# Kernel optimization log

Measured on AMD Instinct MI355X. Metric: run time of the kernel, lower is better.

The kernel has to match this reference:

```python
import jax, jax.numpy as jnp
import numpy as np

D_MODEL = 512
EPS = 1e-5


def setup_inputs() -> dict:
    key = jax.random.key(0)
    k1, k2, k3 = jax.random.split(key, 3)
    B, N, D = 8, 2048, D_MODEL
    output = jax.random.normal(k1, (B, N, D), dtype=jnp.float32)
    # multiplicative 0/1 float mask over the [B, N, N] score matrix
    slf_attn_mask = jax.random.randint(k2, (B, N, N), 0, 2).astype(jnp.float32)
    # nn.Linear(d_model, d_model): weight [out, in], xavier-uniform; bias zeros-ish
    limit = float(np.sqrt(6.0 / (D + D)))
    W = jax.random.uniform(k3, (D, D), dtype=jnp.float32, minval=-limit, maxval=limit)
    b = jnp.zeros((D,), dtype=jnp.float32)
    return {"output": output, "slf_attn_mask": slf_attn_mask, "W": W, "b": b}


def reference(output, slf_attn_mask, W, b):
    temperature = jnp.asarray(D_MODEL, output.dtype) ** 0.5
    # scores: [B, N, N] = (q / temp) @ k^T, then multiplicative mask
    attn = jnp.einsum("bnd,bmd->bnm", output / temperature, output) * slf_attn_mask
    # F.normalize(p=2, dim=-1, eps=1e-5): x / max(||x||_2, eps)
    norm = jnp.sqrt(jnp.sum(attn * attn, axis=-1, keepdims=True))
    attn = attn / jnp.maximum(norm, EPS)
    # values: elu(Linear(output)), Linear uses W @ x + b with W [out, in]
    v = jax.nn.elu(jnp.einsum("bnd,ed->bne", output, W) + b)
    return jnp.einsum("bnm,bme->bne", attn, v)
```

## Files before the change

### kernel.cpp

```cpp
#include <hip/hip_runtime.h>
#include <hip/hip_bf16.h>

#define NSEQ 2048
#define DM 512
#define BATCH 8
#define GTOT (BATCH * NSEQ)
#define INV_T 0.044194173824159216f
#define EPSN 1e-5f

typedef __bf16 bf16_t;
typedef bf16_t bf16x8 __attribute__((ext_vector_type(8)));
typedef float f32x16 __attribute__((ext_vector_type(16)));
typedef unsigned short u16;
typedef unsigned int u32;

__device__ __forceinline__ u16 f2bf(float f) {
    u32 u = __builtin_bit_cast(u32, f);
    u32 r = (u + 0x7FFFu + ((u >> 16) & 1u)) >> 16;
    return (u16)r;
}

__device__ __forceinline__ void async16(const u16* g, u16* l) {
    __builtin_amdgcn_global_load_lds(
        (const __attribute__((address_space(1))) u32*)g,
        (__attribute__((address_space(3))) u32*)l, 16, 0, 0);
}

__device__ __forceinline__ bf16x8 fragld(const u16* t, int row, int kc) {
    return *(const bf16x8*)(t + row * 32 + ((kc ^ ((row >> 1) & 3)) << 3));
}

#define MFMA32(a, b, c) __builtin_amdgcn_mfma_f32_32x32x16_bf16(a, b, c, 0, 0, 0)
#define ROWOFF(reg, lh) (((reg) & 3) + 8 * ((reg) >> 2) + 4 * (lh))

#define STAGE(Ag, ldA, Bg, ldB, k0)                                              \
    do {                                                                         \
        async16((Ag) + (long)rA0 * (ldA) + (k0) + kcg * 8, Ab + u0 * 512 + lane * 8);        \
        async16((Ag) + (long)(rA0 + 16) * (ldA) + (k0) + kcg * 8, Ab + (u0 + 1) * 512 + lane * 8); \
        async16((Bg) + (long)rA0 * (ldB) + (k0) + kcg * 8, Bb + u0 * 512 + lane * 8);        \
        async16((Bg) + (long)(rA0 + 16) * (ldB) + (k0) + kcg * 8, Bb + (u0 + 1) * 512 + lane * 8); \
    } while (0)

__global__ __launch_bounds__(256) void k_convert(
    const float* __restrict__ X, const float* __restrict__ W,
    u16* __restrict__ Kbf, u16* __restrict__ Wbf, float* __restrict__ ssbuf) {
    const long NK = (long)GTOT * DM / 4;
    const long NW = (long)DM * DM / 4;
    const long NS = GTOT / 4;
    long i = (long)blockIdx.x * 256 + threadIdx.x;
    if (i < NK) {
        float4 f = ((const float4*)X)[i];
        ushort4 o;
        o.x = f2bf(f.x); o.y = f2bf(f.y); o.z = f2bf(f.z); o.w = f2bf(f.w);
        ((ushort4*)Kbf)[i] = o;
    } else if (i < NK + NW) {
        long j = i - NK;
        float4 f = ((const float4*)W)[j];
        ushort4 o;
        o.x = f2bf(f.x); o.y = f2bf(f.y); o.z = f2bf(f.z); o.w = f2bf(f.w);
        ((ushort4*)Wbf)[j] = o;
    } else if (i < NK + NW + NS) {
        ((float4*)ssbuf)[i - NK - NW] = (float4){0.f, 0.f, 0.f, 0.f};
    }
}

__global__ __launch_bounds__(256, 4) void k_vgemm(
    const u16* __restrict__ Wbf, const u16* __restrict__ Kbf,
    const float* __restrict__ bias, u16* __restrict__ vT) {
    __shared__ __attribute__((aligned(16))) u16 Ab[4096], Bb[4096];
    const int tid = threadIdx.x, wave = tid >> 6, lane = tid & 63;
    const int l31 = lane & 31, lh = lane >> 5;
    const int wy = wave >> 1, wx = wave & 1;
    const int M0 = blockIdx.y * 128, N0 = blockIdx.x * 128;
    const u16* Ag = Wbf + (long)M0 * DM;
    const u16* Bg = Kbf + (long)N0 * DM;

    const int u0 = wave * 2;
    const int rA0 = u0 * 16 + (lane >> 2);
    const int kcg = (lane & 3) ^ ((lane >> 3) & 3);

    f32x16 acc[2][2];
#pragma unroll
    for (int i = 0; i < 2; ++i)
#pragma unroll
        for (int j = 0; j < 2; ++j)
#pragma unroll
            for (int e = 0; e < 16; ++e) acc[i][j][e] = 0.f;

    for (int kt = 0; kt < 16; ++kt) {
        const int k0 = kt * 32;
        __syncthreads();
        STAGE(Ag, DM, Bg, DM, k0);
        __syncthreads();
#pragma unroll
        for (int ks = 0; ks < 2; ++ks) {
            int kc = ks * 2 + lh;
            bf16x8 a0 = fragld(Ab, wy * 64 + l31, kc);
            bf16x8 a1 = fragld(Ab, wy * 64 + 32 + l31, kc);
            bf16x8 b0 = fragld(Bb, wx * 64 + l31, kc);
            bf16x8 b1 = fragld(Bb, wx * 64 + 32 + l31, kc);
            acc[0][0] = MFMA32(a0, b0, acc[0][0]);
            acc[0][1] = MFMA32(a0, b1, acc[0][1]);
            acc[1][0] = MFMA32(a1, b0, acc[1][0]);
            acc[1][1] = MFMA32(a1, b1, acc[1][1]);
        }
    }
#pragma unroll
    for (int mi = 0; mi < 2; ++mi) {
#pragma unroll
        for (int reg = 0; reg < 16; ++reg) {
            int e = M0 + wy * 64 + mi * 32 + ROWOFF(reg, lh);
            float bv = bias[e];
#pragma unroll
            for (int ni = 0; ni < 2; ++ni) {
                int g = N0 + wx * 64 + ni * 32 + l31;
                float x = acc[mi][ni][reg] + bv;
                float v = x > 0.f ? x : (__expf(x) - 1.f);
                vT[(long)e * GTOT + g] = f2bf(v);
            }
        }
    }
}

__global__ __launch_bounds__(256, 4) void k_sgemm(
    const u16* __restrict__ Kbf, const float* __restrict__ mask,
    u16* __restrict__ Sbuf, float* __restrict__ ssbuf) {
    __shared__ __attribute__((aligned(16))) u16 Ab[4096], Bb[4096];
    const int tid = threadIdx.x, wave = tid >> 6, lane = tid & 63;
    const int l31 = lane & 31, lh = lane >> 5;
    const int wy = wave >> 1, wx = wave & 1;
    const int b = blockIdx.z;
    const int M0 = blockIdx.y * 128, N0 = blockIdx.x * 128;
    const u16* Ag = Kbf + (long)(b * NSEQ + M0) * DM;
    const u16* Bg = Kbf + (long)(b * NSEQ + N0) * DM;

    const int u0 = wave * 2;
    const int rA0 = u0 * 16 + (lane >> 2);
    const int kcg = (lane & 3) ^ ((lane >> 3) & 3);

    f32x16 acc[2][2];
#pragma unroll
    for (int i = 0; i < 2; ++i)
#pragma unroll
        for (int j = 0; j < 2; ++j)
#pragma unroll
            for (int e = 0; e < 16; ++e) acc[i][j][e] = 0.f;

    for (int kt = 0; kt < 16; ++kt) {
        const int k0 = kt * 32;
        __syncthreads();
        STAGE(Ag, DM, Bg, DM, k0);
        __syncthreads();
#pragma unroll
        for (int ks = 0; ks < 2; ++ks) {
            int kc = ks * 2 + lh;
            bf16x8 a0 = fragld(Ab, wy * 64 + l31, kc);
            bf16x8 a1 = fragld(Ab, wy * 64 + 32 + l31, kc);
            bf16x8 b0 = fragld(Bb, wx * 64 + l31, kc);
            bf16x8 b1 = fragld(Bb, wx * 64 + 32 + l31, kc);
            acc[0][0] = MFMA32(a0, b0, acc[0][0]);
            acc[0][1] = MFMA32(a0, b1, acc[0][1]);
            acc[1][0] = MFMA32(a1, b0, acc[1][0]);
            acc[1][1] = MFMA32(a1, b1, acc[1][1]);
        }
    }
#pragma unroll
    for (int mi = 0; mi < 2; ++mi) {
#pragma unroll
        for (int reg = 0; reg < 16; ++reg) {
            long rg = (long)b * NSEQ + M0 + wy * 64 + mi * 32 + ROWOFF(reg, lh);
            float v = 0.f;
#pragma unroll
            for (int ni = 0; ni < 2; ++ni) {
                int cg = N0 + wx * 64 + ni * 32 + l31;
                float s = acc[mi][ni][reg] * INV_T * mask[rg * NSEQ + cg];
                v += s * s;
                Sbuf[rg * NSEQ + cg] = f2bf(s);
            }
            v += __shfl_xor(v, 1, 32);
            v += __shfl_xor(v, 2, 32);
            v += __shfl_xor(v, 4, 32);
            v += __shfl_xor(v, 8, 32);
            v += __shfl_xor(v, 16, 32);
            if (l31 == 0) atomicAdd(&ssbuf[rg], v);
        }
    }
}

__global__ __launch_bounds__(256, 4) void k_pv(
    const u16* __restrict__ Sbuf, const u16* __restrict__ vT,
    const float* __restrict__ ssbuf, float* __restrict__ Out) {
    __shared__ __attribute__((aligned(16))) u16 Ab[4096], Bb[4096];
    __shared__ float sc[128];
    const int tid = threadIdx.x, wave = tid >> 6, lane = tid & 63;
    const int l31 = lane & 31, lh = lane >> 5;
    const int wy = wave >> 1, wx = wave & 1;
    const int b = blockIdx.z;
    const int M0 = blockIdx.y * 128, N0 = blockIdx.x * 128;
    const u16* Ag = Sbuf + (long)(b * NSEQ + M0) * NSEQ;
    const u16* Bg = vT + (long)N0 * GTOT + b * NSEQ;

    if (tid < 128) {
        float v = ssbuf[b * NSEQ + M0 + tid];
        sc[tid] = 1.f / fmaxf(sqrtf(v), EPSN);
    }

    const int u0 = wave * 2;
    const int rA0 = u0 * 16 + (lane >> 2);
    const int kcg = (lane & 3) ^ ((lane >> 3) & 3);

    f32x16 acc[2][2];
#pragma unroll
    for (int i = 0; i < 2; ++i)
#pragma unroll
        for (int j = 0; j < 2; ++j)
#pragma unroll
            for (int e = 0; e < 16; ++e) acc[i][j][e] = 0.f;

    for (int kt = 0; kt < 64; ++kt) {
        const int k0 = kt * 32;
        __syncthreads();
        STAGE(Ag, NSEQ, Bg, GTOT, k0);
        __syncthreads();
#pragma unroll
        for (int ks = 0; ks < 2; ++ks) {
            int kc = ks * 2 + lh;
            bf16x8 a0 = fragld(Ab, wy * 64 + l31, kc);
            bf16x8 a1 = fragld(Ab, wy * 64 + 32 + l31, kc);
            bf16x8 b0 = fragld(Bb, wx * 64 + l31, kc);
            bf16x8 b1 = fragld(Bb, wx * 64 + 32 + l31, kc);
            acc[0][0] = MFMA32(a0, b0, acc[0][0]);
            acc[0][1] = MFMA32(a0, b1, acc[0][1]);
            acc[1][0] = MFMA32(a1, b0, acc[1][0]);
            acc[1][1] = MFMA32(a1, b1, acc[1][1]);
        }
    }
#pragma unroll
    for (int mi = 0; mi < 2; ++mi) {
#pragma unroll
        for (int reg = 0; reg < 16; ++reg) {
            int rl = wy * 64 + mi * 32 + ROWOFF(reg, lh);
            float s = sc[rl];
            float* op = Out + ((long)b * NSEQ + M0 + rl) * DM;
#pragma unroll
            for (int ni = 0; ni < 2; ++ni) {
                int d = N0 + wx * 64 + ni * 32 + l31;
                op[d] = acc[mi][ni][reg] * s;
            }
        }
    }
}

extern "C" void kernel_launch(void* const* d_in, const int* in_sizes, int n_in,
                              void* d_out, int out_size, void* d_ws, size_t ws_size,
                              hipStream_t stream) {
    const float* X = (const float*)d_in[0];
    const float* mask = (const float*)d_in[1];
    const float* W = (const float*)d_in[2];
    const float* bias = (const float*)d_in[3];
    float* out = (float*)d_out;

    char* ws = (char*)d_ws;
    u16* Kbf = (u16*)ws;
    u16* Wbf = (u16*)(ws + 16777216);
    u16* vT = (u16*)(ws + 17301504);
    u16* Sbuf = (u16*)(ws + 34078720);
    float* ssbuf = (float*)(ws + 101187584);

    k_convert<<<8464, 256, 0, stream>>>(X, W, Kbf, Wbf, ssbuf);
    k_vgemm<<<dim3(128, 4), 256, 0, stream>>>(Wbf, Kbf, bias, vT);
    k_sgemm<<<dim3(16, 16, 8), 256, 0, stream>>>(Kbf, mask, Sbuf, ssbuf);
    k_pv<<<dim3(4, 16, 8), 256, 0, stream>>>(Sbuf, vT, ssbuf, out);
}
```

Measured before the change: 354.4 us.

## Double-buffer LDS staging in all GEMMs and enlarge score GEMM tiles

Every GEMM kernel now uses two LDS buffers. The next K-slice is loaded asynchronously while MFMAs run on the current one, which cuts the per-iteration barrier pair down to a single barrier. The score GEMM also moves from 128x128 tiles with 256 threads to 256x256 tiles with 512 threads, where each wave computes four by two MFMA blocks, so K tiles are reused more and global traffic drops. The cost is much larger LDS use (64KB per sgemm block) and more accumulator registers, which lowers occupancy.

```diff
diff --git a/kernel.cpp b/kernel.cpp
--- a/kernel.cpp
+++ b/kernel.cpp
@@ -32,14 +32,6 @@
 
 #define MFMA32(a, b, c) __builtin_amdgcn_mfma_f32_32x32x16_bf16(a, b, c, 0, 0, 0)
 #define ROWOFF(reg, lh) (((reg) & 3) + 8 * ((reg) >> 2) + 4 * (lh))
-
-#define STAGE(Ag, ldA, Bg, ldB, k0)                                              \
-    do {                                                                         \
-        async16((Ag) + (long)rA0 * (ldA) + (k0) + kcg * 8, Ab + u0 * 512 + lane * 8);        \
-        async16((Ag) + (long)(rA0 + 16) * (ldA) + (k0) + kcg * 8, Ab + (u0 + 1) * 512 + lane * 8); \
-        async16((Bg) + (long)rA0 * (ldB) + (k0) + kcg * 8, Bb + u0 * 512 + lane * 8);        \
-        async16((Bg) + (long)(rA0 + 16) * (ldB) + (k0) + kcg * 8, Bb + (u0 + 1) * 512 + lane * 8); \
-    } while (0)
 
 __global__ __launch_bounds__(256) void k_convert(
     const float* __restrict__ X, const float* __restrict__ W,
@@ -64,111 +56,72 @@
     }
 }
 
-__global__ __launch_bounds__(256, 4) void k_vgemm(
-    const u16* __restrict__ Wbf, const u16* __restrict__ Kbf,
-    const float* __restrict__ bias, u16* __restrict__ vT) {
-    __shared__ __attribute__((aligned(16))) u16 Ab[4096], Bb[4096];
+__global__ __launch_bounds__(512, 4) void k_sgemm(
+    const u16* __restrict__ Kbf, const float* __restrict__ mask,
+    u16* __restrict__ Sbuf, float* __restrict__ ssbuf) {
+    __shared__ __attribute__((aligned(16))) u16 Ab[2][8192], Bb[2][8192];
     const int tid = threadIdx.x, wave = tid >> 6, lane = tid & 63;
     const int l31 = lane & 31, lh = lane >> 5;
-    const int wy = wave >> 1, wx = wave & 1;
-    const int M0 = blockIdx.y * 128, N0 = blockIdx.x * 128;
-    const u16* Ag = Wbf + (long)M0 * DM;
-    const u16* Bg = Kbf + (long)N0 * DM;
+    const int wy = wave >> 2, wx = wave & 3;
+    const int b = blockIdx.z;
+    const int M0 = blockIdx.y * 256, N0 = blockIdx.x * 256;
+    const u16* Ag = Kbf + (long)(b * NSEQ + M0) * DM;
+    const u16* Bg = Kbf + (long)(b * NSEQ + N0) * DM;
 
     const int u0 = wave * 2;
     const int rA0 = u0 * 16 + (lane >> 2);
     const int kcg = (lane & 3) ^ ((lane >> 3) & 3);
-
-    f32x16 acc[2][2];
-#pragma unroll
-    for (int i = 0; i < 2; ++i)
+    const long aoff = (long)rA0 * DM + kcg * 8;
+    const int ldst = u0 * 512 + lane * 8;
+
+    f32x16 acc[4][2];
+#pragma unroll
+    for (int i = 0; i < 4; ++i)
 #pragma unroll
         for (int j = 0; j < 2; ++j)
 #pragma unroll
             for (int e = 0; e < 16; ++e) acc[i][j][e] = 0.f;
 
+    async16(Ag + aoff, Ab[0] + ldst);
+    async16(Ag + aoff + 16 * DM, Ab[0] + ldst + 512);
+    async16(Bg + aoff, Bb[0] + ldst);
+    async16(Bg + aoff + 16 * DM, Bb[0] + ldst + 512);
+    __syncthreads();
+
     for (int kt = 0; kt < 16; ++kt) {
-        const int k0 = kt * 32;
-        __syncthreads();
-        STAGE(Ag, DM, Bg, DM, k0);
-        __syncthreads();
+        const int cur = kt & 1, nxt = cur ^ 1;
+        if (kt < 15) {
+            const long o = aoff + (kt + 1) * 32;
+            async16(Ag + o, Ab[nxt] + ldst);
+            async16(Ag + o + 16 * DM, Ab[nxt] + ldst + 512);
+            async16(Bg + o, Bb[nxt] + ldst);
+            async16(Bg + o + 16 * DM, Bb[nxt] + ldst + 512);
+        }
 #pragma unroll
         for (int ks = 0; ks < 2; ++ks) {
-            int kc = ks * 2 + lh;
-            bf16x8 a0 = fragld(Ab, wy * 64 + l31, kc);
-            bf16x8 a1 = fragld(Ab, wy * 64 + 32 + l31, kc);
-            bf16x8 b0 = fragld(Bb, wx * 64 + l31, kc);
-            bf16x8 b1 = fragld(Bb, wx * 64 + 32 + l31, kc);
+            const int kc = ks * 2 + lh;
+            bf16x8 a0 = fragld(Ab[cur], wy * 128 + l31, kc);
+            bf16x8 a1 = fragld(Ab[cur], wy * 128 + 32 + l31, kc);
+            bf16x8 a2 = fragld(Ab[cur], wy * 128 + 64 + l31, kc);
+            bf16x8 a3 = fragld(Ab[cur], wy * 128 + 96 + l31, kc);
+            bf16x8 b0 = fragld(Bb[cur], wx * 64 + l31, kc);
+            bf16x8 b1 = fragld(Bb[cur], wx * 64 + 32 + l31, kc);
             acc[0][0] = MFMA32(a0, b0, acc[0][0]);
             acc[0][1] = MFMA32(a0, b1, acc[0][1]);
             acc[1][0] = MFMA32(a1, b0, acc[1][0]);
             acc[1][1] = MFMA32(a1, b1, acc[1][1]);
-        }
-    }
-#pragma unroll
-    for (int mi = 0; mi < 2; ++mi) {
+            acc[2][0] = MFMA32(a2, b0, acc[2][0]);
+            acc[2][1] = MFMA32(a2, b1, acc[2][1]);
+            acc[3][0] = MFMA32(a3, b0, acc[3][0]);
+            acc[3][1] = MFMA32(a3, b1, acc[3][1]);
+        }
+        __syncthreads();
+    }
+#pragma unroll
+    for (int mi = 0; mi < 4; ++mi) {
 #pragma unroll
         for (int reg = 0; reg < 16; ++reg) {
-            int e = M0 + wy * 64 + mi * 32 + ROWOFF(reg, lh);
-            float bv = bias[e];
-#pragma unroll
-            for (int ni = 0; ni < 2; ++ni) {
-                int g = N0 + wx * 64 + ni * 32 + l31;
-                float x = acc[mi][ni][reg] + bv;
-                float v = x > 0.f ? x : (__expf(x) - 1.f);
-                vT[(long)e * GTOT + g] = f2bf(v);
-            }
-        }
-    }
-}
-
-__global__ __launch_bounds__(256, 4) void k_sgemm(
-    const u16* __restrict__ Kbf, const float* __restrict__ mask,
-    u16* __restrict__ Sbuf, float* __restrict__ ssbuf) {
-    __shared__ __attribute__((aligned(16))) u16 Ab[4096], Bb[4096];
-    const int tid = threadIdx.x, wave = tid >> 6, lane = tid & 63;
-    const int l31 = lane & 31, lh = lane >> 5;
-    const int wy = wave >> 1, wx = wave & 1;
-    const int b = blockIdx.z;
-    const int M0 = blockIdx.y * 128, N0 = blockIdx.x * 128;
-    const u16* Ag = Kbf + (long)(b * NSEQ + M0) * DM;
-    const u16* Bg = Kbf + (long)(b * NSEQ + N0) * DM;
-
-    const int u0 = wave * 2;
-    const int rA0 = u0 * 16 + (lane >> 2);
-    const int kcg = (lane & 3) ^ ((lane >> 3) & 3);
-
-    f32x16 acc[2][2];
-#pragma unroll
-    for (int i = 0; i < 2; ++i)
-#pragma unroll
-        for (int j = 0; j < 2; ++j)
-#pragma unroll
-            for (int e = 0; e < 16; ++e) acc[i][j][e] = 0.f;
-
-    for (int kt = 0; kt < 16; ++kt) {
-        const int k0 = kt * 32;
-        __syncthreads();
-        STAGE(Ag, DM, Bg, DM, k0);
-        __syncthreads();
-#pragma unroll
-        for (int ks = 0; ks < 2; ++ks) {
-            int kc = ks * 2 + lh;
-            bf16x8 a0 = fragld(Ab, wy * 64 + l31, kc);
-            bf16x8 a1 = fragld(Ab, wy * 64 + 32 + l31, kc);
-            bf16x8 b0 = fragld(Bb, wx * 64 + l31, kc);
-            bf16x8 b1 = fragld(Bb, wx * 64 + 32 + l31, kc);
-            acc[0][0] = MFMA32(a0, b0, acc[0][0]);
-            acc[0][1] = MFMA32(a0, b1, acc[0][1]);
-            acc[1][0] = MFMA32(a1, b0, acc[1][0]);
-            acc[1][1] = MFMA32(a1, b1, acc[1][1]);
-        }
-    }
-#pragma unroll
-    for (int mi = 0; mi < 2; ++mi) {
-#pragma unroll
-        for (int reg = 0; reg < 16; ++reg) {
-            long rg = (long)b * NSEQ + M0 + wy * 64 + mi * 32 + ROWOFF(reg, lh);
+            long rg = (long)b * NSEQ + M0 + wy * 128 + mi * 32 + ROWOFF(reg, lh);
             float v = 0.f;
 #pragma unroll
             for (int ni = 0; ni < 2; ++ni) {
@@ -187,10 +140,81 @@
     }
 }
 
+__global__ __launch_bounds__(256, 4) void k_vgemm(
+    const u16* __restrict__ Wbf, const u16* __restrict__ Kbf,
+    const float* __restrict__ bias, u16* __restrict__ vT) {
+    __shared__ __attribute__((aligned(16))) u16 Ab[2][4096], Bb[2][4096];
+    const int tid = threadIdx.x, wave = tid >> 6, lane = tid & 63;
+    const int l31 = lane & 31, lh = lane >> 5;
+    const int wy = wave >> 1, wx = wave & 1;
+    const int M0 = blockIdx.y * 128, N0 = blockIdx.x * 128;
+    const u16* Ag = Wbf + (long)M0 * DM;
+    const u16* Bg = Kbf + (long)N0 * DM;
+
+    const int u0 = wave * 2;
+    const int rA0 = u0 * 16 + (lane >> 2);
+    const int kcg = (lane & 3) ^ ((lane >> 3) & 3);
+    const long aoff = (long)rA0 * DM + kcg * 8;
+    const int ldst = u0 * 512 + lane * 8;
+
+    f32x16 acc[2][2];
+#pragma unroll
+    for (int i = 0; i < 2; ++i)
+#pragma unroll
+        for (int j = 0; j < 2; ++j)
+#pragma unroll
+            for (int e = 0; e < 16; ++e) acc[i][j][e] = 0.f;
+
+    async16(Ag + aoff, Ab[0] + ldst);
+    async16(Ag + aoff + 16 * DM, Ab[0] + ldst + 512);
+    async16(Bg + aoff, Bb[0] + ldst);
+    async16(Bg + aoff + 16 * DM, Bb[0] + ldst + 512);
+    __syncthreads();
+
+    for (int kt = 0; kt < 16; ++kt) {
+        const int cur = kt & 1, nxt = cur ^ 1;
+        if (kt < 15) {
+            const long o = aoff + (kt + 1) * 32;
+            async16(Ag + o, Ab[nxt] + ldst);
+            async16(Ag + o + 16 * DM, Ab[nxt] + ldst + 512);
+            async16(Bg + o, Bb[nxt] + ldst);
+            async16(Bg + o + 16 * DM, Bb[nxt] + ldst + 512);
+        }
+#pragma unroll
+        for (int ks = 0; ks < 2; ++ks) {
+            const int kc = ks * 2 + lh;
+            bf16x8 a0 = fragld(Ab[cur], wy * 64 + l31, kc);
+            bf16x8 a1 = fragld(Ab[cur], wy * 64 + 32 + l31, kc);
+            bf16x8 b0 = fragld(Bb[cur], wx * 64 + l31, kc);
+            bf16x8 b1 = fragld(Bb[cur], wx * 64 + 32 + l31, kc);
+            acc[0][0] = MFMA32(a0, b0, acc[0][0]);
+            acc[0][1] = MFMA32(a0, b1, acc[0][1]);
+            acc[1][0] = MFMA32(a1, b0, acc[1][0]);
+            acc[1][1] = MFMA32(a1, b1, acc[1][1]);
+        }
+        __syncthreads();
+    }
+#pragma unroll
+    for (int mi = 0; mi < 2; ++mi) {
+#pragma unroll
+        for (int reg = 0; reg < 16; ++reg) {
+            int e = M0 + wy * 64 + mi * 32 + ROWOFF(reg, lh);
+            float bv = bias[e];
+#pragma unroll
+            for (int ni = 0; ni < 2; ++ni) {
+                int g = N0 + wx * 64 + ni * 32 + l31;
+                float x = acc[mi][ni][reg] + bv;
+                float v = x > 0.f ? x : (__expf(x) - 1.f);
+                vT[(long)e * GTOT + g] = f2bf(v);
+            }
+        }
+    }
+}
+
 __global__ __launch_bounds__(256, 4) void k_pv(
     const u16* __restrict__ Sbuf, const u16* __restrict__ vT,
     const float* __restrict__ ssbuf, float* __restrict__ Out) {
-    __shared__ __attribute__((aligned(16))) u16 Ab[4096], Bb[4096];
+    __shared__ __attribute__((aligned(16))) u16 Ab[2][4096], Bb[2][4096];
     __shared__ float sc[128];
     const int tid = threadIdx.x, wave = tid >> 6, lane = tid & 63;
     const int l31 = lane & 31, lh = lane >> 5;
@@ -208,6 +232,9 @@
     const int u0 = wave * 2;
     const int rA0 = u0 * 16 + (lane >> 2);
     const int kcg = (lane & 3) ^ ((lane >> 3) & 3);
+    const long aoff = (long)rA0 * NSEQ + kcg * 8;
+    const long boff = (long)rA0 * GTOT + kcg * 8;
+    const int ldst = u0 * 512 + lane * 8;
 
     f32x16 acc[2][2];
 #pragma unroll
@@ -217,23 +244,35 @@
 #pragma unroll
             for (int e = 0; e < 16; ++e) acc[i][j][e] = 0.f;
 
+    async16(Ag + aoff, Ab[0] + ldst);
+    async16(Ag + aoff + 16 * NSEQ, Ab[0] + ldst + 512);
+    async16(Bg + boff, Bb[0] + ldst);
+    async16(Bg + boff + 16 * GTOT, Bb[0] + ldst + 512);
+    __syncthreads();
+
     for (int kt = 0; kt < 64; ++kt) {
-        const int k0 = kt * 32;
-        __syncthreads();
-        STAGE(Ag, NSEQ, Bg, GTOT, k0);
-        __syncthreads();
+        const int cur = kt & 1, nxt = cur ^ 1;
+        if (kt < 63) {
+            const long oa = aoff + (kt + 1) * 32;
+            const long ob = boff + (kt + 1) * 32;
+            async16(Ag + oa, Ab[nxt] + ldst);
+            async16(Ag + oa + 16 * NSEQ, Ab[nxt] + ldst + 512);
+            async16(Bg + ob, Bb[nxt] + ldst);
+            async16(Bg + ob + 16 * GTOT, Bb[nxt] + ldst + 512);
+        }
 #pragma unroll
         for (int ks = 0; ks < 2; ++ks) {
-            int kc = ks * 2 + lh;
-            bf16x8 a0 = fragld(Ab, wy * 64 + l31, kc);
-            bf16x8 a1 = fragld(Ab, wy * 64 + 32 + l31, kc);
-            bf16x8 b0 = fragld(Bb, wx * 64 + l31, kc);
-            bf16x8 b1 = fragld(Bb, wx * 64 + 32 + l31, kc);
+            const int kc = ks * 2 + lh;
+            bf16x8 a0 = fragld(Ab[cur], wy * 64 + l31, kc);
+            bf16x8 a1 = fragld(Ab[cur], wy * 64 + 32 + l31, kc);
+            bf16x8 b0 = fragld(Bb[cur], wx * 64 + l31, kc);
+            bf16x8 b1 = fragld(Bb[cur], wx * 64 + 32 + l31, kc);
             acc[0][0] = MFMA32(a0, b0, acc[0][0]);
             acc[0][1] = MFMA32(a0, b1, acc[0][1]);
             acc[1][0] = MFMA32(a1, b0, acc[1][0]);
             acc[1][1] = MFMA32(a1, b1, acc[1][1]);
         }
+        __syncthreads();
     }
 #pragma unroll
     for (int mi = 0; mi < 2; ++mi) {
@@ -269,6 +308,6 @@
 
     k_convert<<<8464, 256, 0, stream>>>(X, W, Kbf, Wbf, ssbuf);
     k_vgemm<<<dim3(128, 4), 256, 0, stream>>>(Wbf, Kbf, bias, vT);
-    k_sgemm<<<dim3(16, 16, 8), 256, 0, stream>>>(Kbf, mask, Sbuf, ssbuf);
+    k_sgemm<<<dim3(8, 8, 8), 512, 0, stream>>>(Kbf, mask, Sbuf, ssbuf);
     k_pv<<<dim3(4, 16, 8), 256, 0, stream>>>(Sbuf, vT, ssbuf, out);
 }
```

After: 978.2 us. 2.76x slower.
